# Performance work log

Measured on AMD Instinct MI355X. Metric: run time of the kernel, lower is better.

The kernel has to match this reference:

```python
import jax, jax.numpy as jnp
import numpy as np

C0, C1, C2 = 2000, 10000, 50000  # class cutoffs
D = 1024                          # input_size (hidden dim)
OUT_HEAD = C0 + 2                 # head output: shortlist + 2 cluster logits


def setup_inputs() -> dict:
    key = jax.random.key(0)
    ks = jax.random.split(key, 7)
    s = lambda fan_in: 1.0 / np.sqrt(fan_in)
    x = jax.random.normal(ks[0], (4096, D), dtype=jnp.float32)
    Wh = jax.random.normal(ks[1], (OUT_HEAD, D), dtype=jnp.float32) * s(D)
    bh = jnp.zeros((OUT_HEAD,), dtype=jnp.float32)
    # tail 0: D -> D//4**0 -> (C1-C0)
    W0a = jax.random.normal(ks[2], (D, D), dtype=jnp.float32) * s(D)
    W0b = jax.random.normal(ks[3], (C1 - C0, D), dtype=jnp.float32) * s(D)
    # tail 1: D -> D//4**1 -> (C2-C1)
    W1a = jax.random.normal(ks[4], (D // 4, D), dtype=jnp.float32) * s(D)
    W1b = jax.random.normal(ks[5], (C2 - C1, D // 4), dtype=jnp.float32) * s(D // 4)
    return {"x": x, "Wh": Wh, "bh": bh, "W0a": W0a, "W0b": W0b, "W1a": W1a, "W1b": W1b}


def reference(x, Wh, bh, W0a, W0b, W1a, W1b):
    # head: [B, OUT_HEAD]; log-softmax over shortlist + cluster logits
    lsm_head = jax.nn.log_softmax(x @ Wh.T + bh, axis=-1)
    # tail clusters: capacity-reduction linear, projection, log-softmax within cluster
    lsm_t0 = jax.nn.log_softmax((x @ W0a.T) @ W0b.T, axis=-1)  # [B, C1-C0]
    lsm_t1 = jax.nn.log_softmax((x @ W1a.T) @ W1b.T, axis=-1)  # [B, C2-C1]
    # flat log-probs: cluster log-prob broadcast-added to within-cluster log-probs
    prob = jnp.concatenate([
        lsm_head[:, :C0],
        lsm_head[:, C0:C0 + 1] + lsm_t0,
        lsm_head[:, C0 + 1:C0 + 2] + lsm_t1,
    ], axis=1)  # [B, C2]
    return prob
```

## Files before the change

kernel.cpp:

```cpp
#include <hip/hip_runtime.h>
#include <hip/hip_bf16.h>
#include <math.h>

#define CC0 2000
#define CC1 10000
#define CC2 50000
#define DH  1024
#define BATCH 4096
#define OUT_HEAD (CC0 + 2)

#define N0_P 8192
#define N1_P 40192
#define NH_P 2048

typedef __attribute__((ext_vector_type(4))) float  f32x4;
typedef __attribute__((ext_vector_type(8))) __bf16 bf16x8;
typedef __attribute__((ext_vector_type(8))) short  s16x8;

__device__ __forceinline__ void gload_lds16(const void* g, void* l) {
    __builtin_amdgcn_global_load_lds(
        (const __attribute__((address_space(1))) void*)g,
        (__attribute__((address_space(3))) void*)l, 16, 0, 0);
}

__global__ __launch_bounds__(256) void convert_all_kernel(
    const float4* __restrict__ s0, ushort4* __restrict__ d0, int n0s, int n0d,
    const float4* __restrict__ s1, ushort4* __restrict__ d1, int n1s, int n1d,
    const float4* __restrict__ s2, ushort4* __restrict__ d2, int n2s, int n2d,
    const float4* __restrict__ s3, ushort4* __restrict__ d3, int n3s, int n3d,
    const float4* __restrict__ s4, ushort4* __restrict__ d4, int n4s, int n4d,
    const float4* __restrict__ s5, ushort4* __restrict__ d5, int n5s, int n5d)
{
    const float4* src; ushort4* dst; int ns, nd;
    switch (blockIdx.y) {
        case 0: src = s0; dst = d0; ns = n0s; nd = n0d; break;
        case 1: src = s1; dst = d1; ns = n1s; nd = n1d; break;
        case 2: src = s2; dst = d2; ns = n2s; nd = n2d; break;
        case 3: src = s3; dst = d3; ns = n3s; nd = n3d; break;
        case 4: src = s4; dst = d4; ns = n4s; nd = n4d; break;
        default: src = s5; dst = d5; ns = n5s; nd = n5d; break;
    }
    int i = blockIdx.x * blockDim.x + threadIdx.x;
    const int stride = gridDim.x * blockDim.x;
    for (; i < nd; i += stride) {
        ushort4 o = {0, 0, 0, 0};
        if (i < ns) {
            float4 v = src[i];
            o.x = __builtin_bit_cast(unsigned short, (__bf16)v.x);
            o.y = __builtin_bit_cast(unsigned short, (__bf16)v.y);
            o.z = __builtin_bit_cast(unsigned short, (__bf16)v.z);
            o.w = __builtin_bit_cast(unsigned short, (__bf16)v.w);
        }
        dst[i] = o;
    }
}

__global__ __launch_bounds__(256) void gemm128x3_kernel(
    const ushort* __restrict__ x_bf,
    const ushort* __restrict__ W0a_bf, ushort* __restrict__ h0,
    const ushort* __restrict__ W1a_bf, ushort* __restrict__ h1,
    const ushort* __restrict__ Wh_bf,  float*  __restrict__ headL)
{
    __shared__ ushort As[128 * 64];
    __shared__ ushort Bs[128 * 64];

    const int gb = blockIdx.x;
    const ushort* B; void* C;
    int N, ldC, wmode, nbx, lin;
    const int K = DH;
    if (gb < 256)      { B = W0a_bf; C = h0;    N = DH;       ldC = DH;       wmode = 1; nbx = 8;  lin = gb; }
    else if (gb < 320) { B = W1a_bf; C = h1;    N = 256;      ldC = 256;      wmode = 1; nbx = 2;  lin = gb - 256; }
    else               { B = Wh_bf;  C = headL; N = OUT_HEAD; ldC = OUT_HEAD; wmode = 2; nbx = 16; lin = gb - 320; }

    const int nwg = nbx * 32;
    const int q = nwg >> 3;
    int bid = (lin & 7) * q + (lin >> 3);
    const int bx = bid % nbx;
    const int by = bid / nbx;

    const int t = threadIdx.x;
    const int lane = t & 63;
    const int w = t >> 6;
    const int wr = w >> 1, wc = w & 1;
    const int lr = lane & 15;
    const int lg = lane >> 4;
    const int bm = by * 128;
    const int bn = bx * 128;
    const int lrow = lane >> 3;
    const int lcol = (lane & 7) * 8;

    f32x4 acc[4][4] = {};

    for (int k0 = 0; k0 < K; k0 += 64) {
        #pragma unroll
        for (int i = 0; i < 4; ++i) {
            const int seg = w * 4 + i;
            const int row = seg * 8 + lrow;
            gload_lds16(x_bf + (size_t)(bm + row) * K + k0 + lcol, &As[seg * 512]);
            gload_lds16(B + (size_t)(bn + row) * K + k0 + lcol, &Bs[seg * 512]);
        }
        __syncthreads();
        #pragma unroll
        for (int ks = 0; ks < 2; ++ks) {
            s16x8 af[4], bfr[4];
            #pragma unroll
            for (int m = 0; m < 4; ++m)
                af[m] = *(const s16x8*)&As[(wr * 64 + m * 16 + lr) * 64 + ks * 32 + lg * 8];
            #pragma unroll
            for (int n = 0; n < 4; ++n)
                bfr[n] = *(const s16x8*)&Bs[(wc * 64 + n * 16 + lr) * 64 + ks * 32 + lg * 8];
            #pragma unroll
            for (int m = 0; m < 4; ++m)
                #pragma unroll
                for (int n = 0; n < 4; ++n)
                    acc[m][n] = __builtin_amdgcn_mfma_f32_16x16x32_bf16(
                        __builtin_bit_cast(bf16x8, af[m]),
                        __builtin_bit_cast(bf16x8, bfr[n]), acc[m][n], 0, 0, 0);
        }
        __syncthreads();
    }

    #pragma unroll
    for (int m = 0; m < 4; ++m)
        #pragma unroll
        for (int r = 0; r < 4; ++r) {
            const int row = bm + wr * 64 + m * 16 + lg * 4 + r;
            #pragma unroll
            for (int n = 0; n < 4; ++n) {
                const int col = bn + wc * 64 + n * 16 + lr;
                float v = acc[m][n][r];
                if (col < N) {
                    if (wmode == 1)
                        ((ushort*)C)[(size_t)row * ldC + col] =
                            __builtin_bit_cast(unsigned short, (__bf16)v);
                    else
                        ((float*)C)[(size_t)row * ldC + col] = v;
                }
            }
        }
}

__global__ __launch_bounds__(512, 1) void tails256_kernel(
    const ushort* __restrict__ h0, const ushort* __restrict__ W0b,
    ushort* __restrict__ L0,
    const ushort* __restrict__ h1, const ushort* __restrict__ W1b,
    ushort* __restrict__ L1)
{
    __shared__ ushort lds[2][2][256 * 64];

    const int gb = blockIdx.x;
    const ushort *A, *B; ushort* C;
    int K, N, nbx, ldC, lin;
    if (gb < 512) { A = h0; B = W0b; C = L0; K = DH;  N = CC1 - CC0; nbx = N0_P / 256; ldC = N0_P; lin = gb; }
    else          { A = h1; B = W1b; C = L1; K = 256; N = CC2 - CC1; nbx = N1_P / 256; ldC = N1_P; lin = gb - 512; }

    const int nwg = nbx * 16;
    const int q8 = nwg >> 3;
    int bid = (lin & 7) * q8 + (lin >> 3);
    const int by = bid % 16;
    const int bx = bid / 16;
    const int bm = by * 256, bn = bx * 256;

    const int t = threadIdx.x;
    const int lane = t & 63;
    const int w = t >> 6;
    const int wr = w >> 2;
    const int wc = w & 3;
    const int lr = lane & 15;
    const int lg = lane >> 4;
    const int xr = (lr & 7) << 4;
    const int c0 = w * 64 + lane;

    f32x4 acc[8][4] = {};
    const int nkt = K / 64;

    auto stage_chunk = [&](int ktile, int buf, int p) {
        const int k0 = ktile * 64;
        const int mat = (p == 1 || p == 2) ? 1 : 0;
        const int j = (p == 3) ? 1 : (p == 2 ? 1 : 0);
        const ushort* gbase = mat ? B : A;
        const int brow = mat ? bn : bm;
        #pragma unroll
        for (int i = 0; i < 2; ++i) {
            const int v = i * 512 + c0;
            const int vrow = v >> 3;
            int ar;
            if (mat == 0) ar = ((vrow >> 6) << 7) + (j << 6) + (vrow & 63);
            else          ar = ((vrow >> 5) << 6) + (j << 5) + (vrow & 31);
            const int cc = (v & 7) ^ (ar & 7);
            const int v0 = (i * 512 + w * 64) >> 3;
            int ar0;
            if (mat == 0) ar0 = ((v0 >> 6) << 7) + (j << 6) + (v0 & 63);
            else          ar0 = ((v0 >> 5) << 6) + (j << 5) + (v0 & 31);
            gload_lds16(gbase + (size_t)(brow + ar) * K + k0 + cc * 8,
                        (char*)&lds[buf][mat][0] + ar0 * 128);
        }
    };

    #pragma unroll
    for (int p = 0; p < 4; ++p) stage_chunk(0, 0, p);
    asm volatile("s_waitcnt vmcnt(0)" ::: "memory");
    __builtin_amdgcn_s_barrier();
    asm volatile("" ::: "memory");

    for (int tk = 0; tk < nkt; ++tk) {
        const int cur = tk & 1;
        const char* baseA = (const char*)&lds[cur][0][0];
        const char* baseB = (const char*)&lds[cur][1][0];
        const bool more = (tk + 1 < nkt);

        s16x8 bq[4][2];
        s16x8 af[4][2];

        #pragma unroll
        for (int p = 0; p < 4; ++p) {
            const int mh = p >> 1, nh = p & 1;
            if (more) {
                stage_chunk(tk + 1, cur ^ 1, p);
                asm volatile("s_waitcnt vmcnt(6)" ::: "memory");
            } else {
                if (p == 0)      asm volatile("s_waitcnt vmcnt(4)" ::: "memory");
                else if (p == 1) asm volatile("s_waitcnt vmcnt(2)" ::: "memory");
                else if (p == 2) asm volatile("s_waitcnt vmcnt(0)" ::: "memory");
            }
            __builtin_amdgcn_s_barrier();
            asm volatile("" ::: "memory");

            if (p == 0 || p == 2) {
                #pragma unroll
                for (int m_ = 0; m_ < 4; ++m_) {
                    const int row = wr * 128 + (mh * 4 + m_) * 16 + lr;
                    #pragma unroll
                    for (int ks = 0; ks < 2; ++ks)
                        af[m_][ks] = *(const s16x8*)(baseA + (row * 128 + ((ks * 64 + lg * 16) ^ xr)));
                }
            }
            if (p == 0 || p == 1) {
                #pragma unroll
                for (int n_ = 0; n_ < 2; ++n_) {
                    const int row = wc * 64 + (p * 2 + n_) * 16 + lr;
                    #pragma unroll
                    for (int ks = 0; ks < 2; ++ks)
                        bq[p * 2 + n_][ks] = *(const s16x8*)(baseB + (row * 128 + ((ks * 64 + lg * 16) ^ xr)));
                }
            }
            __builtin_amdgcn_s_setprio(1);
            #pragma unroll
            for (int m_ = 0; m_ < 4; ++m_)
                #pragma unroll
                for (int n_ = 0; n_ < 2; ++n_)
                    #pragma unroll
                    for (int ks = 0; ks < 2; ++ks)
                        acc[mh * 4 + m_][nh * 2 + n_] = __builtin_amdgcn_mfma_f32_16x16x32_bf16(
                            __builtin_bit_cast(bf16x8, af[m_][ks]),
                            __builtin_bit_cast(bf16x8, bq[nh * 2 + n_][ks]),
                            acc[mh * 4 + m_][nh * 2 + n_], 0, 0, 0);
            __builtin_amdgcn_s_setprio(0);
        }
    }

    #pragma unroll
    for (int m = 0; m < 8; ++m) {
        #pragma unroll
        for (int r = 0; r < 4; ++r) {
            const int row = bm + wr * 128 + m * 16 + lg * 4 + r;
            #pragma unroll
            for (int n = 0; n < 4; ++n) {
                const int col = bn + wc * 64 + n * 16 + lr;
                if (col < N)
                    C[(size_t)row * ldC + col] =
                        __builtin_bit_cast(unsigned short, (__bf16)acc[m][n][r]);
            }
        }
    }
}

__global__ __launch_bounds__(256) void head_lsm_kernel(
    const float* __restrict__ HL, const float* __restrict__ bh,
    float* __restrict__ out, float* __restrict__ s01)
{
    const int row = blockIdx.x;
    const float* L = HL + (size_t)row * OUT_HEAD;
    const int t = threadIdx.x;
    __shared__ float red[4];

    float m = -1e30f;
    for (int i = t; i < OUT_HEAD; i += 256) m = fmaxf(m, L[i] + bh[i]);
    #pragma unroll
    for (int s = 1; s < 64; s <<= 1) m = fmaxf(m, __shfl_xor(m, s, 64));
    if ((t & 63) == 0) red[t >> 6] = m;
    __syncthreads();
    m = fmaxf(fmaxf(red[0], red[1]), fmaxf(red[2], red[3]));

    float sum = 0.f;
    for (int i = t; i < OUT_HEAD; i += 256) sum += __expf(L[i] + bh[i] - m);
    #pragma unroll
    for (int s = 1; s < 64; s <<= 1) sum += __shfl_xor(sum, s, 64);
    __syncthreads();
    if ((t & 63) == 0) red[t >> 6] = sum;
    __syncthreads();
    const float lse = m + logf(red[0] + red[1] + red[2] + red[3]);

    float* orow = out + (size_t)row * CC2;
    for (int i = t; i < CC0; i += 256) orow[i] = L[i] + bh[i] - lse;
    if (t == 0) {
        s01[2 * row + 0] = L[CC0 + 0] + bh[CC0 + 0] - lse;
        s01[2 * row + 1] = L[CC0 + 1] + bh[CC0 + 1] - lse;
    }
}

__global__ __launch_bounds__(512) void finalize_rows_kernel(
    const ushort* __restrict__ L0, const ushort* __restrict__ L1,
    const float* __restrict__ s01, float* __restrict__ out)
{
    const int row = blockIdx.x;
    const int t = threadIdx.x;
    const ushort* r0 = L0 + (size_t)row * N0_P;
    const ushort* r1 = L1 + (size_t)row * N1_P;

    float p0 = 0.f, p1 = 0.f;
    for (int c = t; c < 1000; c += 512) {
        s16x8 v = *(const s16x8*)(r0 + c * 8);
        #pragma unroll
        for (int j = 0; j < 8; ++j)
            p0 += __expf(__builtin_bit_cast(float, (unsigned)(unsigned short)v[j] << 16));
    }
    for (int c = t; c < 5000; c += 512) {
        s16x8 v = *(const s16x8*)(r1 + c * 8);
        #pragma unroll
        for (int j = 0; j < 8; ++j)
            p1 += __expf(__builtin_bit_cast(float, (unsigned)(unsigned short)v[j] << 16));
    }
    #pragma unroll
    for (int s = 1; s < 64; s <<= 1) {
        p0 += __shfl_xor(p0, s, 64);
        p1 += __shfl_xor(p1, s, 64);
    }
    __shared__ float red0[8], red1[8], bc[2];
    if ((t & 63) == 0) { red0[t >> 6] = p0; red1[t >> 6] = p1; }
    __syncthreads();
    if (t == 0) {
        float s0 = 0.f, s1 = 0.f;
        #pragma unroll
        for (int i = 0; i < 8; ++i) { s0 += red0[i]; s1 += red1[i]; }
        bc[0] = s01[2 * row + 0] - logf(s0);
        bc[1] = s01[2 * row + 1] - logf(s1);
    }
    __syncthreads();
    const float a0 = bc[0], a1 = bc[1];

    float* o = out + (size_t)row * CC2;
    for (int c = t; c < 6000; c += 512) {
        const bool t0 = c < 1000;
        const ushort* src = t0 ? r0 + c * 8 : r1 + (size_t)(c - 1000) * 8;
        float* dst = t0 ? o + CC0 + c * 8 : o + CC1 + (c - 1000) * 8;
        const float add = t0 ? a0 : a1;
        s16x8 v = *(const s16x8*)src;
        float4 o0, o1;
        o0.x = __builtin_bit_cast(float, (unsigned)(unsigned short)v[0] << 16) + add;
        o0.y = __builtin_bit_cast(float, (unsigned)(unsigned short)v[1] << 16) + add;
        o0.z = __builtin_bit_cast(float, (unsigned)(unsigned short)v[2] << 16) + add;
        o0.w = __builtin_bit_cast(float, (unsigned)(unsigned short)v[3] << 16) + add;
        o1.x = __builtin_bit_cast(float, (unsigned)(unsigned short)v[4] << 16) + add;
        o1.y = __builtin_bit_cast(float, (unsigned)(unsigned short)v[5] << 16) + add;
        o1.z = __builtin_bit_cast(float, (unsigned)(unsigned short)v[6] << 16) + add;
        o1.w = __builtin_bit_cast(float, (unsigned)(unsigned short)v[7] << 16) + add;
        *(float4*)dst = o0;
        *(float4*)(dst + 4) = o1;
    }
}

extern "C" void kernel_launch(void* const* d_in, const int* in_sizes, int n_in,
                              void* d_out, int out_size, void* d_ws, size_t ws_size,
                              hipStream_t stream) {
    const float* x   = (const float*)d_in[0];
    const float* Wh  = (const float*)d_in[1];
    const float* bh  = (const float*)d_in[2];
    const float* W0a = (const float*)d_in[3];
    const float* W0b = (const float*)d_in[4];
    const float* W1a = (const float*)d_in[5];
    const float* W1b = (const float*)d_in[6];
    float* out = (float*)d_out;
    char*  ws  = (char*)d_ws;

    size_t off = 0;
    auto alloc = [&](size_t bytes) { size_t o = off; off += (bytes + 255) & ~(size_t)255; return o; };
    ushort* x_bf   = (ushort*)(ws + alloc((size_t)BATCH * DH * 2));
    ushort* Wh_bf  = (ushort*)(ws + alloc((size_t)NH_P * DH * 2));
    ushort* W0a_bf = (ushort*)(ws + alloc((size_t)DH * DH * 2));
    ushort* W0b_bf = (ushort*)(ws + alloc((size_t)N0_P * DH * 2));
    ushort* W1a_bf = (ushort*)(ws + alloc((size_t)256 * DH * 2));
    ushort* W1b_bf = (ushort*)(ws + alloc((size_t)N1_P * 256 * 2));
    ushort* h0_bf  = (ushort*)(ws + alloc((size_t)BATCH * DH * 2));
    ushort* h1_bf  = (ushort*)(ws + alloc((size_t)BATCH * 256 * 2));
    float*  headL  = (float*)(ws + alloc((size_t)BATCH * OUT_HEAD * 4));
    float*  s01    = (float*)(ws + alloc((size_t)BATCH * 2 * 4));
    ushort* L0     = (ushort*)(ws + alloc((size_t)BATCH * N0_P * 2));
    ushort* L1     = (ushort*)(ws + alloc((size_t)BATCH * N1_P * 2));

    convert_all_kernel<<<dim3(1280, 6), 256, 0, stream>>>(
        (const float4*)x,   (ushort4*)x_bf,   BATCH * DH / 4,        BATCH * DH / 4,
        (const float4*)Wh,  (ushort4*)Wh_bf,  OUT_HEAD * DH / 4,     NH_P * DH / 4,
        (const float4*)W0a, (ushort4*)W0a_bf, DH * DH / 4,           DH * DH / 4,
        (const float4*)W0b, (ushort4*)W0b_bf, (CC1 - CC0) * DH / 4,  N0_P * DH / 4,
        (const float4*)W1a, (ushort4*)W1a_bf, 256 * DH / 4,          256 * DH / 4,
        (const float4*)W1b, (ushort4*)W1b_bf, (CC2 - CC1) * 256 / 4, N1_P * 256 / 4);

    gemm128x3_kernel<<<832, 256, 0, stream>>>(
        x_bf, W0a_bf, h0_bf, W1a_bf, h1_bf, Wh_bf, headL);

    head_lsm_kernel<<<BATCH, 256, 0, stream>>>(headL, bh, out, s01);

    tails256_kernel<<<512 + (N1_P / 256) * 16, 512, 0, stream>>>(
        h0_bf, W0b_bf, L0, h1_bf, W1b_bf, L1);

    finalize_rows_kernel<<<BATCH, 512, 0, stream>>>(L0, L1, s01, out);
}
```

Before: 600.4 us.

## Keep W1b tile resident in LDS and sweep 8 row-blocks per tail-1 workgroup

The tail-1 GEMM (K=256) path gets its own code path. Each workgroup loads its full 256-column W1b slice (all of K) into LDS once, then loops over 8 row blocks of 128 rows, streaming A fragments directly from global memory into registers with double buffering. This replaces the generic 256x256 double-buffered LDS pipeline, whose staging and barrier overhead is poorly amortised over only 4 k-tiles. The grid for this part changes from 2512 to 628 workgroups. The cost is less LDS reuse of A, since h1 is now read from global/L2 per wave, and fewer workgroups available for latency hiding.

```diff
diff --git a/kernel.cpp b/kernel.cpp
--- a/kernel.cpp
+++ b/kernel.cpp
@@ -146,13 +146,112 @@
     const ushort* __restrict__ h1, const ushort* __restrict__ W1b,
     ushort* __restrict__ L1)
 {
-    __shared__ ushort lds[2][2][256 * 64];
+    __shared__ ushort lds[4][256 * 64];
 
     const int gb = blockIdx.x;
-    const ushort *A, *B; ushort* C;
-    int K, N, nbx, ldC, lin;
-    if (gb < 512) { A = h0; B = W0b; C = L0; K = DH;  N = CC1 - CC0; nbx = N0_P / 256; ldC = N0_P; lin = gb; }
-    else          { A = h1; B = W1b; C = L1; K = 256; N = CC2 - CC1; nbx = N1_P / 256; ldC = N1_P; lin = gb - 512; }
+    const int t = threadIdx.x;
+    const int lane = t & 63;
+    const int w = t >> 6;
+    const int lr = lane & 15;
+    const int lg = lane >> 4;
+    const int xr = (lr & 7) << 4;
+    const int c0 = w * 64 + lane;
+
+    if (gb >= 512) {
+        const int lin = gb - 512;
+        const int p  = lin >> 2;
+        const int mg = lin & 3;
+        const int bn = p * 256;
+        const int wr = w >> 2;
+        const int wc = w & 3;
+        ushort* ldsf = &lds[0][0];
+
+        #pragma unroll
+        for (int kt = 0; kt < 4; ++kt) {
+            #pragma unroll
+            for (int j = 0; j < 2; ++j) {
+                #pragma unroll
+                for (int i = 0; i < 2; ++i) {
+                    const int v = i * 512 + c0;
+                    const int vrow = v >> 3;
+                    const int ar = ((vrow >> 5) << 6) + (j << 5) + (vrow & 31);
+                    const int cc = (v & 7) ^ (ar & 7);
+                    const int v0 = (i * 512 + w * 64) >> 3;
+                    const int ar0 = ((v0 >> 5) << 6) + (j << 5) + (v0 & 31);
+                    gload_lds16(W1b + (size_t)(bn + ar) * 256 + kt * 64 + cc * 8,
+                                (char*)(ldsf + kt * 256 * 64) + ar0 * 128);
+                }
+            }
+        }
+        asm volatile("s_waitcnt vmcnt(0)" ::: "memory");
+        __builtin_amdgcn_s_barrier();
+        asm volatile("" ::: "memory");
+
+        for (int s = 0; s < 8; ++s) {
+            const int bmS = (mg * 8 + s) * 128;
+            const ushort* Abase = h1 + (size_t)(bmS + wr * 64 + lr) * 256 + lg * 8;
+
+            s16x8 afb[2][4][2];
+            #pragma unroll
+            for (int m_ = 0; m_ < 4; ++m_)
+                #pragma unroll
+                for (int ks = 0; ks < 2; ++ks)
+                    afb[0][m_][ks] = *(const s16x8*)(Abase + (size_t)(m_ * 16) * 256 + ks * 32);
+
+            f32x4 acc[4][4] = {};
+            #pragma unroll
+            for (int kt = 0; kt < 4; ++kt) {
+                if (kt < 3) {
+                    #pragma unroll
+                    for (int m_ = 0; m_ < 4; ++m_)
+                        #pragma unroll
+                        for (int ks = 0; ks < 2; ++ks)
+                            afb[(kt + 1) & 1][m_][ks] =
+                                *(const s16x8*)(Abase + (size_t)(m_ * 16) * 256 + (kt + 1) * 64 + ks * 32);
+                }
+                const char* baseB = (const char*)(ldsf + kt * 256 * 64);
+                s16x8 bq[4][2];
+                #pragma unroll
+                for (int n_ = 0; n_ < 4; ++n_) {
+                    const int row = wc * 64 + n_ * 16 + lr;
+                    #pragma unroll
+                    for (int ks = 0; ks < 2; ++ks)
+                        bq[n_][ks] = *(const s16x8*)(baseB + (row * 128 + ((ks * 64 + lg * 16) ^ xr)));
+                }
+                __builtin_amdgcn_s_setprio(1);
+                #pragma unroll
+                for (int m_ = 0; m_ < 4; ++m_)
+                    #pragma unroll
+                    for (int n_ = 0; n_ < 4; ++n_)
+                        #pragma unroll
+                        for (int ks = 0; ks < 2; ++ks)
+                            acc[m_][n_] = __builtin_amdgcn_mfma_f32_16x16x32_bf16(
+                                __builtin_bit_cast(bf16x8, afb[kt & 1][m_][ks]),
+                                __builtin_bit_cast(bf16x8, bq[n_][ks]),
+                                acc[m_][n_], 0, 0, 0);
+                __builtin_amdgcn_s_setprio(0);
+            }
+
+            #pragma unroll
+            for (int m = 0; m < 4; ++m)
+                #pragma unroll
+                for (int r = 0; r < 4; ++r) {
+                    const int row = bmS + wr * 64 + m * 16 + lg * 4 + r;
+                    #pragma unroll
+                    for (int n = 0; n < 4; ++n) {
+                        const int col = bn + wc * 64 + n * 16 + lr;
+                        if (col < CC2 - CC1)
+                            L1[(size_t)row * N1_P + col] =
+                                __builtin_bit_cast(unsigned short, (__bf16)acc[m][n][r]);
+                    }
+                }
+        }
+        return;
+    }
+
+    const ushort* A = h0; const ushort* B = W0b; ushort* C = L0;
+    const int K = DH, N = CC1 - CC0, nbx = N0_P / 256, ldC = N0_P;
+    const int lin = gb;
 
     const int nwg = nbx * 16;
     const int q8 = nwg >> 3;
@@ -160,16 +259,10 @@
     const int by = bid % 16;
     const int bx = bid / 16;
     const int bm = by * 256, bn = bx * 256;
-
-    const int t = threadIdx.x;
-    const int lane = t & 63;
-    const int w = t >> 6;
     const int wr = w >> 2;
     const int wc = w & 3;
-    const int lr = lane & 15;
-    const int lg = lane >> 4;
-    const int xr = (lr & 7) << 4;
-    const int c0 = w * 64 + lane;
+
+    ushort (*lds2)[2][256 * 64] = (ushort (*)[2][256 * 64])lds;
 
     f32x4 acc[8][4] = {};
     const int nkt = K / 64;
@@ -193,7 +286,7 @@
             if (mat == 0) ar0 = ((v0 >> 6) << 7) + (j << 6) + (v0 & 63);
             else          ar0 = ((v0 >> 5) << 6) + (j << 5) + (v0 & 31);
             gload_lds16(gbase + (size_t)(brow + ar) * K + k0 + cc * 8,
-                        (char*)&lds[buf][mat][0] + ar0 * 128);
+                        (char*)&lds2[buf][mat][0] + ar0 * 128);
         }
     };
 
@@ -205,8 +298,8 @@
 
     for (int tk = 0; tk < nkt; ++tk) {
         const int cur = tk & 1;
-        const char* baseA = (const char*)&lds[cur][0][0];
-        const char* baseB = (const char*)&lds[cur][1][0];
+        const char* baseA = (const char*)&lds2[cur][0][0];
+        const char* baseB = (const char*)&lds2[cur][1][0];
         const bool more = (tk + 1 < nkt);
 
         s16x8 bq[4][2];
@@ -411,7 +504,7 @@
 
     head_lsm_kernel<<<BATCH, 256, 0, stream>>>(headL, bh, out, s01);
 
-    tails256_kernel<<<512 + (N1_P / 256) * 16, 512, 0, stream>>>(
+    tails256_kernel<<<512 + 628, 512, 0, stream>>>(
         h0_bf, W0b_bf, L0, h1_bf, W1b_bf, L1);
 
     finalize_rows_kernel<<<BATCH, 512, 0, stream>>>(L0, L1, s01, out);
```

Measured after the change: 706.0 us. 17.6% more time.
